# Kernel tuning notes

Measured on AMD Instinct MI355X. Metric: run time of the kernel, lower is better.

The kernel has to match this reference:

```python
import jax, jax.numpy as jnp
import numpy as np

B, C = 1, 1
D = H = W = 128          # volume depth/height/width (z, y, x)
V = U = 128              # detector rows (v) / cols (u)
A = 96                   # projection angles
N_STEPS = 128            # Joseph ray-marching steps
SX = SY = SD = 1.0       # voxel size (sd, sy, sx)
SU = SV = 1.0            # detector spacing (sv, su)


def setup_inputs() -> dict:
    key = jax.random.key(0)
    # model-facing volume [B, C, X, Y, Z]
    vol = jax.random.normal(key, (B, C, W, H, D), dtype=jnp.float32)
    angles = jnp.linspace(0.0, np.pi, A, endpoint=False).astype(jnp.float32)
    return {"vol": vol, "angles": angles}


def _corner(idx, size):
    """Floor/ceil corner indices + zero-padded linear weights (align_corners=True,
    padding_mode='zeros' semantics of F.grid_sample)."""
    i0f = jnp.floor(idx)
    frac = idx - i0f
    i0 = i0f.astype(jnp.int32)
    i1 = i0 + 1
    w0 = jnp.where((i0 >= 0) & (i0 < size), 1.0 - frac, 0.0)
    w1 = jnp.where((i1 >= 0) & (i1 < size), frac, 0.0)
    return jnp.clip(i0, 0, size - 1), jnp.clip(i1, 0, size - 1), w0, w1


def reference(vol, angles):
    # [B,C,X,Y,Z] -> [B,C,D,H,W] (z,y,x ordering used internally)
    v_zyx = jnp.transpose(vol, (0, 1, 4, 3, 2))
    cos_t = jnp.cos(angles)[:, None]   # [A,1]
    sin_t = jnp.sin(angles)[:, None]   # [A,1]
    u = (jnp.arange(U, dtype=jnp.float32) - (U - 1) / 2.0) * SU   # [U]
    v = (jnp.arange(V, dtype=jnp.float32) - (V - 1) / 2.0) * SV   # [V]
    # half ray length = half in-plane diagonal
    T = 0.5 * float(np.sqrt(((W - 1) * SX) ** 2 + ((H - 1) * SY) ** 2))
    delta_t = 2.0 * T / float(N_STEPS)

    x_base = -u[None, :] * sin_t   # [A,U] ray point at t=0
    y_base = u[None, :] * cos_t    # [A,U]
    # z depends only on detector row v; constant along the ray
    z_idx = v / SD + (D - 1) / 2.0                     # [V]
    z0, z1, wz0, wz1 = _corner(z_idx, D)
    z0, z1 = z0[:, None], z1[:, None]                  # [V,1]
    wz0, wz1 = wz0[:, None], wz1[:, None]

    t_vals = -T + (jnp.arange(N_STEPS, dtype=jnp.float32) + 0.5) * delta_t

    def step(acc, t):
        x_idx = (x_base + t * cos_t) / SX + (W - 1) / 2.0   # [A,U]
        y_idx = (y_base + t * sin_t) / SY + (H - 1) / 2.0   # [A,U]
        x0, x1, wx0, wx1 = [a[:, None, :] for a in _corner(x_idx, W)]  # [A,1,U]
        y0, y1, wy0, wy1 = [a[:, None, :] for a in _corner(y_idx, H)]  # [A,1,U]
        g = lambda zi, yi, xi: v_zyx[:, :, zi, yi, xi]      # -> [B,C,A,V,U]
        s = (wz0 * (wy0 * (wx0 * g(z0, y0, x0) + wx1 * g(z0, y0, x1))
                    + wy1 * (wx0 * g(z0, y1, x0) + wx1 * g(z0, y1, x1)))
             + wz1 * (wy0 * (wx0 * g(z1, y0, x0) + wx1 * g(z1, y0, x1))
                      + wy1 * (wx0 * g(z1, y1, x0) + wx1 * g(z1, y1, x1))))
        return acc + s, None

    acc0 = jnp.zeros((B, C, A, V, U), dtype=vol.dtype)
    acc, _ = jax.lax.scan(jax.checkpoint(step), acc0, t_vals)
    sino = acc * jnp.float32(delta_t)            # [B,C,A,V,U]
    # model-facing sinogram [B,C,X=U,A,Z=V]
    return jnp.transpose(sino, (0, 1, 4, 2, 3))
```

## Files before the change

### kernel.cpp

```cpp
#include <hip/hip_runtime.h>
#include <hip/hip_fp16.h>

namespace {
constexpr int A_N = 96;
constexpr int U_N = 128;
constexpr int V_N = 128;
constexpr int W_N = 128;
constexpr int H_N = 128;
constexpr int NSTEPS = 128;
constexpr float T_HALF = 89.80256121069154f;
constexpr float DT = 1.4031650189170554f;
constexpr float INV_DT = 1.0f / DT;
constexpr int PAD = 6;
constexpr int WP = W_N + 2 * PAD;
constexpr int ROW_BYTES = WP * 256;
constexpr int ZT = 8;
constexpr int RAYS_PER_WAVE = 8;
constexpr int RAYS_PER_BLOCK = 16;
constexpr int BLOCK_THREADS = 256;
constexpr size_t VOLP_COLS = (size_t)WP * WP;
constexpr size_t VOLP_BYTES = VOLP_COLS * 256;
constexpr size_t SINO = (size_t)U_N * A_N * V_N;
}

typedef __attribute__((ext_vector_type(4))) unsigned int u32x4;

__device__ __forceinline__ unsigned int packh2(float a, float b) {
    return (unsigned int)__half_as_ushort(__float2half_rn(a)) |
           ((unsigned int)__half_as_ushort(__float2half_rn(b)) << 16);
}

__global__ __launch_bounds__(256) void vol_pad_f16(
    const float* __restrict__ vol, unsigned int* __restrict__ volp)
{
    const int idx = blockIdx.x * 256 + threadIdx.x;
    if (idx >= (int)(VOLP_COLS * 16)) return;
    const int zo  = idx & 15;
    const int col = idx >> 4;
    const int yp = col % WP;
    const int xp = col / WP;
    const int x = xp - PAD;
    const int y = yp - PAD;
    uint4 o = make_uint4(0u, 0u, 0u, 0u);
    if ((unsigned)x < 128u && (unsigned)y < 128u) {
        const float* src = vol + (((size_t)x * 128 + y) << 7) + zo * 8;
        const float4 f0 = *(const float4*)(src);
        const float4 f1 = *(const float4*)(src + 4);
        o.x = packh2(f0.x, f0.y);
        o.y = packh2(f0.z, f0.w);
        o.z = packh2(f1.x, f1.y);
        o.w = packh2(f1.z, f1.w);
    }
    *(uint4*)((char*)volp + (size_t)col * 256 + zo * 16) = o;
}

#define ISSUE4(p, q0, q1, q2, q3)                                        \
    asm volatile("global_load_dwordx4 %0, %4, off\n\t"                   \
                 "global_load_dwordx4 %1, %4, off offset:128\n\t"        \
                 "global_load_dwordx4 %2, %4, off offset:256\n\t"        \
                 "global_load_dwordx4 %3, %4, off offset:384"            \
                 : "=&v"(q0), "=&v"(q1), "=&v"(q2), "=&v"(q3)            \
                 : "v"(p))

#define WAIT_VM8()  do { asm volatile("s_waitcnt vmcnt(8)" ::: "memory"); \
                         __builtin_amdgcn_sched_barrier(0); } while (0)
#define WAIT_VM0()  do { asm volatile("s_waitcnt vmcnt(0)" ::: "memory"); \
                         __builtin_amdgcn_sched_barrier(0); } while (0)

__global__ __launch_bounds__(BLOCK_THREADS, 4) void joseph_fwd_fused(
    const unsigned short* __restrict__ volp,
    const float* __restrict__ angles,
    float* __restrict__ out)
{
    const int zo = threadIdx.x & (ZT - 1);
    const int rw = (threadIdx.x >> 3) & 7;
    const int wv = threadIdx.x >> 6;
    const int ray = (wv & 1) * 8 + rw;
    const int shalf = wv >> 1;

    const int lin = (int)blockIdx.x + 8 * (int)blockIdx.y;
    const int swz = (lin & 7) * 96 + (lin >> 3);
    const int a   = swz >> 3;
    const int xtr = swz & 7;
    const int xt = (xtr & 1) ? (4 + (xtr >> 1)) : (3 - (xtr >> 1));
    const int u_i = xt * RAYS_PER_BLOCK + ray;

    const int i0 = shalf * (NSTEPS / 2);
    const int i1 = i0 + NSTEPS / 2;

    const float ang = angles[a];
    const float cv = cosf(ang);
    const float sv = sinf(ang);
    const float up = (float)u_i - 63.5f;
    const float xb = fmaf(-up, sv, 63.5f);
    const float yb = fmaf( up, cv, 63.5f);

    float tlo = -2.f * T_HALF, thi = 2.f * T_HALF;
    if (fabsf(cv) > 1e-6f) {
        const float ta = (-1.f - xb) / cv, tb = (128.f - xb) / cv;
        tlo = fmaxf(tlo, fminf(ta, tb));
        thi = fminf(thi, fmaxf(ta, tb));
    } else if (xb <= -1.f || xb >= 128.f) { thi = tlo - 1.f; }
    if (fabsf(sv) > 1e-6f) {
        const float ta = (-1.f - yb) / sv, tb = (128.f - yb) / sv;
        tlo = fmaxf(tlo, fminf(ta, tb));
        thi = fminf(thi, fmaxf(ta, tb));
    } else if (yb <= -1.f || yb >= 128.f) { thi = tlo - 1.f; }
    const int ilo = (int)floorf(fmaf(tlo + T_HALF, INV_DT, -0.5f)) - 1;
    const int ihi = (int)ceilf (fmaf(thi + T_HALF, INV_DT, -0.5f)) + 1;
    int lo = min(max(ilo, i0), i1);
    int hi = min(max(ihi + 1, i0), i1);
    lo &= ~1;
    hi = (hi + 1) & ~1;

    const char* __restrict__ volc = (const char*)volp;
    const int laneb = zo << 4;

    __half2 hacc[8];
    float accf[16];
#pragma unroll
    for (int j = 0; j < 8; ++j) hacc[j] = __float2half2_rn(0.f);
#pragma unroll
    for (int k = 0; k < 16; ++k) accf[k] = 0.f;

    auto base_of = [&](float i_f, float& fx, float& fy) -> const char* {
        const float tf = fmaf(i_f + 0.5f, DT, -T_HALF);
        const float xi = fmaf(tf, cv, xb);
        const float yi = fmaf(tf, sv, yb);
        const float fx0 = floorf(xi);
        const float fy0 = floorf(yi);
        fx = xi - fx0;
        fy = yi - fy0;
        const int x0 = (int)fx0;
        const int y0 = (int)fy0;
        return volc + ((((x0 + PAD) * WP + (y0 + PAD)) << 8) + laneb);
    };

    auto cons = [&](u32x4 q00l, u32x4 q00h, u32x4 q01l, u32x4 q01h,
                    u32x4 q10l, u32x4 q10h, u32x4 q11l, u32x4 q11h,
                    float fx, float fy) {
        const float wx0 = 1.f - fx;
        const float wy0 = 1.f - fy;
        const __half2 w00 = __float2half2_rn(wx0 * wy0);
        const __half2 w01 = __float2half2_rn(wx0 * fy);
        const __half2 w10 = __float2half2_rn(fx  * wy0);
        const __half2 w11 = __float2half2_rn(fx  * fy);
#pragma unroll
        for (int j = 0; j < 4; ++j) {
            hacc[j] = __hfma2(w00, __builtin_bit_cast(__half2, (unsigned int)q00l[j]), hacc[j]);
            hacc[j] = __hfma2(w01, __builtin_bit_cast(__half2, (unsigned int)q01l[j]), hacc[j]);
            hacc[j] = __hfma2(w10, __builtin_bit_cast(__half2, (unsigned int)q10l[j]), hacc[j]);
            hacc[j] = __hfma2(w11, __builtin_bit_cast(__half2, (unsigned int)q11l[j]), hacc[j]);
            hacc[4 + j] = __hfma2(w00, __builtin_bit_cast(__half2, (unsigned int)q00h[j]), hacc[4 + j]);
            hacc[4 + j] = __hfma2(w01, __builtin_bit_cast(__half2, (unsigned int)q01h[j]), hacc[4 + j]);
            hacc[4 + j] = __hfma2(w10, __builtin_bit_cast(__half2, (unsigned int)q10h[j]), hacc[4 + j]);
            hacc[4 + j] = __hfma2(w11, __builtin_bit_cast(__half2, (unsigned int)q11h[j]), hacc[4 + j]);
        }
    };

    auto flush = [&]() {
#pragma unroll
        for (int j = 0; j < 8; ++j) {
            const float2 f = __half22float2(hacc[j]);
            accf[2 * j]     += f.x;
            accf[2 * j + 1] += f.y;
            hacc[j] = __float2half2_rn(0.f);
        }
    };

    if (lo < hi) {
        u32x4 A0, A1, A2, A3, A4, A5, A6, A7;
        u32x4 B0, B1, B2, B3, B4, B5, B6, B7;
        float fxA, fyA, fxB, fyB;
        int kc = 0;
        int i = lo;
        {
            const char* p  = base_of((float)i, fxA, fyA);
            const char* p2 = p + ROW_BYTES;
            ISSUE4(p,  A0, A1, A2, A3);
            ISSUE4(p2, A4, A5, A6, A7);
        }
        for (;;) {
            {
                const char* p  = base_of((float)(i + 1), fxB, fyB);
                const char* p2 = p + ROW_BYTES;
                ISSUE4(p,  B0, B1, B2, B3);
                ISSUE4(p2, B4, B5, B6, B7);
            }
            WAIT_VM8();
            cons(A0, A1, A2, A3, A4, A5, A6, A7, fxA, fyA);
            i += 2;
            if (i >= hi) {
                WAIT_VM0();
                cons(B0, B1, B2, B3, B4, B5, B6, B7, fxB, fyB);
                break;
            }
            {
                const char* p  = base_of((float)i, fxA, fyA);
                const char* p2 = p + ROW_BYTES;
                ISSUE4(p,  A0, A1, A2, A3);
                ISSUE4(p2, A4, A5, A6, A7);
            }
            WAIT_VM8();
            cons(B0, B1, B2, B3, B4, B5, B6, B7, fxB, fyB);
            if (((++kc) & 1) == 0) flush();
        }
    }
    flush();

    __shared__ float part[RAYS_PER_BLOCK][V_N];
    if (shalf == 1) {
        float* p0 = &part[ray][8 * zo];
        float* p1 = &part[ray][64 + 8 * zo];
        *(float4*)(p0)     = make_float4(accf[0],  accf[1],  accf[2],  accf[3]);
        *(float4*)(p0 + 4) = make_float4(accf[4],  accf[5],  accf[6],  accf[7]);
        *(float4*)(p1)     = make_float4(accf[8],  accf[9],  accf[10], accf[11]);
        *(float4*)(p1 + 4) = make_float4(accf[12], accf[13], accf[14], accf[15]);
    }
    __syncthreads();
    if (shalf == 0) {
        const float* p0 = &part[ray][8 * zo];
        const float* p1 = &part[ray][64 + 8 * zo];
        const float4 q0 = *(const float4*)(p0);
        const float4 q1 = *(const float4*)(p0 + 4);
        const float4 q2 = *(const float4*)(p1);
        const float4 q3 = *(const float4*)(p1 + 4);
        float* op = out + ((size_t)u_i * A_N + a) * V_N;
        float* opl = op + 8 * zo;
        float* oph = op + 64 + 8 * zo;
        *(float4*)(opl)     = make_float4((accf[0]  + q0.x) * DT, (accf[1]  + q0.y) * DT,
                                          (accf[2]  + q0.z) * DT, (accf[3]  + q0.w) * DT);
        *(float4*)(opl + 4) = make_float4((accf[4]  + q1.x) * DT, (accf[5]  + q1.y) * DT,
                                          (accf[6]  + q1.z) * DT, (accf[7]  + q1.w) * DT);
        *(float4*)(oph)     = make_float4((accf[8]  + q2.x) * DT, (accf[9]  + q2.y) * DT,
                                          (accf[10] + q2.z) * DT, (accf[11] + q2.w) * DT);
        *(float4*)(oph + 4) = make_float4((accf[12] + q3.x) * DT, (accf[13] + q3.y) * DT,
                                          (accf[14] + q3.z) * DT, (accf[15] + q3.w) * DT);
    }
}

__global__ __launch_bounds__(256) void joseph_fwd_f32(
    const float* __restrict__ vol,
    const float* __restrict__ angles,
    float* __restrict__ out)
{
    const int zo  = threadIdx.x & 15;
    const int r   = threadIdx.x >> 4;
    const int u_i = blockIdx.x * 16 + r;
    const int a   = blockIdx.y;

    const float ang = angles[a];
    const float c = cosf(ang);
    const float s = sinf(ang);
    const float u = (float)u_i - 63.5f;
    const float xb = fmaf(-u, s, 63.5f);
    const float yb = fmaf( u, c, 63.5f);

    const float* volz = vol + 8 * zo;
    float4 accA = make_float4(0.f, 0.f, 0.f, 0.f);
    float4 accB = make_float4(0.f, 0.f, 0.f, 0.f);

    for (int i = 0; i < NSTEPS; ++i) {
        const float t  = fmaf((float)i + 0.5f, DT, -T_HALF);
        const float xi = fmaf(t, c, xb);
        const float yi = fmaf(t, s, yb);
        const float fx0f = floorf(xi);
        const float fy0f = floorf(yi);
        const int x0 = (int)fx0f;
        const int y0 = (int)fy0f;
        const float fx = xi - fx0f;
        const float fy = yi - fy0f;
        const int x1 = x0 + 1;
        const int y1 = y0 + 1;
        const float wx0 = (x0 >= 0 && x0 < W_N) ? (1.f - fx) : 0.f;
        const float wx1 = (x1 >= 0 && x1 < W_N) ? fx : 0.f;
        const float wy0 = (y0 >= 0 && y0 < H_N) ? (1.f - fy) : 0.f;
        const float wy1 = (y1 >= 0 && y1 < H_N) ? fy : 0.f;
        if ((wx0 + wx1) == 0.f || (wy0 + wy1) == 0.f) continue;
        const int cx0 = min(max(x0, 0), W_N - 1);
        const int cx1 = min(max(x1, 0), W_N - 1);
        const int cy0 = min(max(y0, 0), H_N - 1);
        const int cy1 = min(max(y1, 0), H_N - 1);
        const float* p00 = volz + ((cx0 * H_N + cy0) << 7);
        const float* p01 = volz + ((cx1 * H_N + cy0) << 7);
        const float* p10 = volz + ((cx0 * H_N + cy1) << 7);
        const float* p11 = volz + ((cx1 * H_N + cy1) << 7);
        const float4 v00a = *(const float4*)(p00);
        const float4 v00b = *(const float4*)(p00 + 4);
        const float4 v01a = *(const float4*)(p01);
        const float4 v01b = *(const float4*)(p01 + 4);
        const float4 v10a = *(const float4*)(p10);
        const float4 v10b = *(const float4*)(p10 + 4);
        const float4 v11a = *(const float4*)(p11);
        const float4 v11b = *(const float4*)(p11 + 4);
        const float w00 = wx0 * wy0, w01 = wx1 * wy0, w10 = wx0 * wy1, w11 = wx1 * wy1;
        accA.x = fmaf(w00, v00a.x, fmaf(w01, v01a.x, fmaf(w10, v10a.x, fmaf(w11, v11a.x, accA.x))));
        accA.y = fmaf(w00, v00a.y, fmaf(w01, v01a.y, fmaf(w10, v10a.y, fmaf(w11, v11a.y, accA.y))));
        accA.z = fmaf(w00, v00a.z, fmaf(w01, v01a.z, fmaf(w10, v10a.z, fmaf(w11, v11a.z, accA.z))));
        accA.w = fmaf(w00, v00a.w, fmaf(w01, v01a.w, fmaf(w10, v10a.w, fmaf(w11, v11a.w, accA.w))));
        accB.x = fmaf(w00, v00b.x, fmaf(w01, v01b.x, fmaf(w10, v10b.x, fmaf(w11, v11b.x, accB.x))));
        accB.y = fmaf(w00, v00b.y, fmaf(w01, v01b.y, fmaf(w10, v10b.y, fmaf(w11, v11b.y, accB.y))));
        accB.z = fmaf(w00, v00b.z, fmaf(w01, v01b.z, fmaf(w10, v10b.z, fmaf(w11, v11b.z, accB.z))));
        accB.w = fmaf(w00, v00b.w, fmaf(w01, v01b.w, fmaf(w10, v10b.w, fmaf(w11, v11b.w, accB.w))));
    }

    float* op = out + ((size_t)u_i * A_N + a) * V_N + 8 * zo;
    *(float4*)(op)     = make_float4(accA.x * DT, accA.y * DT, accA.z * DT, accA.w * DT);
    *(float4*)(op + 4) = make_float4(accB.x * DT, accB.y * DT, accB.z * DT, accB.w * DT);
}

extern "C" void kernel_launch(void* const* d_in, const int* in_sizes, int n_in,
                              void* d_out, int out_size, void* d_ws, size_t ws_size,
                              hipStream_t stream) {
    const float* vol    = (const float*)d_in[0];
    const float* angles = (const float*)d_in[1];
    float* out          = (float*)d_out;

    const int pad_blocks = (int)((VOLP_COLS * 16 + 255) / 256);

    if (ws_size >= VOLP_BYTES) {
        unsigned int* volp = (unsigned int*)d_ws;
        hipLaunchKernelGGL(vol_pad_f16, dim3(pad_blocks), dim3(256), 0, stream, vol, volp);
        dim3 grid(U_N / RAYS_PER_BLOCK, A_N);
        hipLaunchKernelGGL(joseph_fwd_fused, grid, dim3(BLOCK_THREADS), 0, stream,
                           (const unsigned short*)volp, angles, out);
    } else {
        dim3 grid(U_N / 16, A_N);
        hipLaunchKernelGGL(joseph_fwd_f32, grid, dim3(256), 0, stream, vol, angles, out);
    }
}
```

Measured before the change: 105.9 us.

## Split ray steps across four waves with interleaved step assignment

Each block now handles 8 rays instead of 16, and the four waves interleave over ray steps (stride 4) instead of two halves covering contiguous step ranges. Step ranges are unioned across the wave via shuffles, and out-of-range steps are masked with a zero weight and clamped addresses. The goal is to balance work between waves, since clipped rays previously left one half idle. The cost is extra masked loads for rays shorter than the wave maximum, a 3-way LDS reduction, and a doubled grid size, which the host launch must match.

```diff
diff --git a/kernel.cpp b/kernel.cpp
--- a/kernel.cpp
+++ b/kernel.cpp
@@ -15,12 +15,12 @@
 constexpr int WP = W_N + 2 * PAD;
 constexpr int ROW_BYTES = WP * 256;
 constexpr int ZT = 8;
-constexpr int RAYS_PER_WAVE = 8;
-constexpr int RAYS_PER_BLOCK = 16;
+constexpr int RAYS_PER_BLOCK = 8;
 constexpr int BLOCK_THREADS = 256;
 constexpr size_t VOLP_COLS = (size_t)WP * WP;
 constexpr size_t VOLP_BYTES = VOLP_COLS * 256;
 constexpr size_t SINO = (size_t)U_N * A_N * V_N;
+constexpr int MAXB = (int)(VOLP_BYTES - ROW_BYTES - 512);
 }
 
 typedef __attribute__((ext_vector_type(4))) unsigned int u32x4;
@@ -73,20 +73,15 @@
     float* __restrict__ out)
 {
     const int zo = threadIdx.x & (ZT - 1);
-    const int rw = (threadIdx.x >> 3) & 7;
+    const int r  = (threadIdx.x >> 3) & 7;
     const int wv = threadIdx.x >> 6;
-    const int ray = (wv & 1) * 8 + rw;
-    const int shalf = wv >> 1;
-
-    const int lin = (int)blockIdx.x + 8 * (int)blockIdx.y;
-    const int swz = (lin & 7) * 96 + (lin >> 3);
-    const int a   = swz >> 3;
-    const int xtr = swz & 7;
-    const int xt = (xtr & 1) ? (4 + (xtr >> 1)) : (3 - (xtr >> 1));
-    const int u_i = xt * RAYS_PER_BLOCK + ray;
-
-    const int i0 = shalf * (NSTEPS / 2);
-    const int i1 = i0 + NSTEPS / 2;
+
+    const int lin = (int)blockIdx.x + 16 * (int)blockIdx.y;
+    const int swz = (lin & 7) * 192 + (lin >> 3);
+    const int a   = swz >> 4;
+    const int xtr = swz & 15;
+    const int xt = (xtr & 1) ? (8 + (xtr >> 1)) : (7 - (xtr >> 1));
+    const int u_i = xt * RAYS_PER_BLOCK + r;
 
     const float ang = angles[a];
     const float cv = cosf(ang);
@@ -108,10 +103,15 @@
     } else if (yb <= -1.f || yb >= 128.f) { thi = tlo - 1.f; }
     const int ilo = (int)floorf(fmaf(tlo + T_HALF, INV_DT, -0.5f)) - 1;
     const int ihi = (int)ceilf (fmaf(thi + T_HALF, INV_DT, -0.5f)) + 1;
-    int lo = min(max(ilo, i0), i1);
-    int hi = min(max(ihi + 1, i0), i1);
-    lo &= ~1;
-    hi = (hi + 1) & ~1;
+    const int lo_r = min(max(ilo, 0), NSTEPS);
+    const int hi_r = min(max(ihi + 1, 0), NSTEPS);
+
+    int lo_w = lo_r, hi_w = hi_r;
+#pragma unroll
+    for (int m = 8; m < 64; m <<= 1) {
+        lo_w = min(lo_w, __shfl_xor(lo_w, m));
+        hi_w = max(hi_w, __shfl_xor(hi_w, m));
+    }
 
     const char* __restrict__ volc = (const char*)volp;
     const int laneb = zo << 4;
@@ -123,28 +123,32 @@
 #pragma unroll
     for (int k = 0; k < 16; ++k) accf[k] = 0.f;
 
-    auto base_of = [&](float i_f, float& fx, float& fy) -> const char* {
-        const float tf = fmaf(i_f + 0.5f, DT, -T_HALF);
+    auto base_of = [&](int i, float& fx, float& fy, float& vf) -> const char* {
+        const float tf = fmaf((float)i + 0.5f, DT, -T_HALF);
         const float xi = fmaf(tf, cv, xb);
         const float yi = fmaf(tf, sv, yb);
         const float fx0 = floorf(xi);
         const float fy0 = floorf(yi);
         fx = xi - fx0;
         fy = yi - fy0;
+        vf = (i >= lo_r && i < hi_r) ? 1.f : 0.f;
         const int x0 = (int)fx0;
         const int y0 = (int)fy0;
-        return volc + ((((x0 + PAD) * WP + (y0 + PAD)) << 8) + laneb);
+        int base = (((x0 + PAD) * WP + (y0 + PAD)) << 8);
+        base = min(max(base, 0), MAXB);
+        return volc + (base + laneb);
     };
 
     auto cons = [&](u32x4 q00l, u32x4 q00h, u32x4 q01l, u32x4 q01h,
                     u32x4 q10l, u32x4 q10h, u32x4 q11l, u32x4 q11h,
-                    float fx, float fy) {
-        const float wx0 = 1.f - fx;
+                    float fx, float fy, float vf) {
+        const float wx0 = (1.f - fx) * vf;
+        const float wx1 = fx * vf;
         const float wy0 = 1.f - fy;
         const __half2 w00 = __float2half2_rn(wx0 * wy0);
         const __half2 w01 = __float2half2_rn(wx0 * fy);
-        const __half2 w10 = __float2half2_rn(fx  * wy0);
-        const __half2 w11 = __float2half2_rn(fx  * fy);
+        const __half2 w10 = __float2half2_rn(wx1 * wy0);
+        const __half2 w11 = __float2half2_rn(wx1 * fy);
 #pragma unroll
         for (int j = 0; j < 4; ++j) {
             hacc[j] = __hfma2(w00, __builtin_bit_cast(__half2, (unsigned int)q00l[j]), hacc[j]);
@@ -168,74 +172,81 @@
         }
     };
 
-    if (lo < hi) {
+    const int i_start = lo_w + ((wv - lo_w) & 3);
+    if (i_start < hi_w) {
+        const int n = (hi_w - i_start + 3) >> 2;
+        const int n_pairs = (n + 1) >> 1;
         u32x4 A0, A1, A2, A3, A4, A5, A6, A7;
         u32x4 B0, B1, B2, B3, B4, B5, B6, B7;
-        float fxA, fyA, fxB, fyB;
-        int kc = 0;
-        int i = lo;
+        float fxA, fyA, vfA, fxB, fyB, vfB;
+        int i = i_start;
+        int k = 0;
         {
-            const char* p  = base_of((float)i, fxA, fyA);
+            const char* p  = base_of(i, fxA, fyA, vfA);
             const char* p2 = p + ROW_BYTES;
             ISSUE4(p,  A0, A1, A2, A3);
             ISSUE4(p2, A4, A5, A6, A7);
         }
         for (;;) {
             {
-                const char* p  = base_of((float)(i + 1), fxB, fyB);
+                const char* p  = base_of(i + 4, fxB, fyB, vfB);
                 const char* p2 = p + ROW_BYTES;
                 ISSUE4(p,  B0, B1, B2, B3);
                 ISSUE4(p2, B4, B5, B6, B7);
             }
             WAIT_VM8();
-            cons(A0, A1, A2, A3, A4, A5, A6, A7, fxA, fyA);
-            i += 2;
-            if (i >= hi) {
+            cons(A0, A1, A2, A3, A4, A5, A6, A7, fxA, fyA, vfA);
+            ++k;
+            if (k == n_pairs) {
                 WAIT_VM0();
-                cons(B0, B1, B2, B3, B4, B5, B6, B7, fxB, fyB);
+                cons(B0, B1, B2, B3, B4, B5, B6, B7, fxB, fyB, vfB);
                 break;
             }
             {
-                const char* p  = base_of((float)i, fxA, fyA);
+                const char* p  = base_of(i + 8, fxA, fyA, vfA);
                 const char* p2 = p + ROW_BYTES;
                 ISSUE4(p,  A0, A1, A2, A3);
                 ISSUE4(p2, A4, A5, A6, A7);
             }
             WAIT_VM8();
-            cons(B0, B1, B2, B3, B4, B5, B6, B7, fxB, fyB);
-            if (((++kc) & 1) == 0) flush();
+            cons(B0, B1, B2, B3, B4, B5, B6, B7, fxB, fyB, vfB);
+            i += 8;
+            if ((k & 1) == 0) flush();
         }
     }
     flush();
 
-    __shared__ float part[RAYS_PER_BLOCK][V_N];
-    if (shalf == 1) {
-        float* p0 = &part[ray][8 * zo];
-        float* p1 = &part[ray][64 + 8 * zo];
+    __shared__ float part[3][RAYS_PER_BLOCK][V_N];
+    if (wv > 0) {
+        float* p0 = &part[wv - 1][r][8 * zo];
+        float* p1 = &part[wv - 1][r][64 + 8 * zo];
         *(float4*)(p0)     = make_float4(accf[0],  accf[1],  accf[2],  accf[3]);
         *(float4*)(p0 + 4) = make_float4(accf[4],  accf[5],  accf[6],  accf[7]);
         *(float4*)(p1)     = make_float4(accf[8],  accf[9],  accf[10], accf[11]);
         *(float4*)(p1 + 4) = make_float4(accf[12], accf[13], accf[14], accf[15]);
     }
     __syncthreads();
-    if (shalf == 0) {
-        const float* p0 = &part[ray][8 * zo];
-        const float* p1 = &part[ray][64 + 8 * zo];
-        const float4 q0 = *(const float4*)(p0);
-        const float4 q1 = *(const float4*)(p0 + 4);
-        const float4 q2 = *(const float4*)(p1);
-        const float4 q3 = *(const float4*)(p1 + 4);
+    if (wv == 0) {
+#pragma unroll
+        for (int w = 0; w < 3; ++w) {
+            const float* p0 = &part[w][r][8 * zo];
+            const float* p1 = &part[w][r][64 + 8 * zo];
+            const float4 q0 = *(const float4*)(p0);
+            const float4 q1 = *(const float4*)(p0 + 4);
+            const float4 q2 = *(const float4*)(p1);
+            const float4 q3 = *(const float4*)(p1 + 4);
+            accf[0] += q0.x;  accf[1] += q0.y;  accf[2]  += q0.z;  accf[3]  += q0.w;
+            accf[4] += q1.x;  accf[5] += q1.y;  accf[6]  += q1.z;  accf[7]  += q1.w;
+            accf[8] += q2.x;  accf[9] += q2.y;  accf[10] += q2.z;  accf[11] += q2.w;
+            accf[12] += q3.x; accf[13] += q3.y; accf[14] += q3.z;  accf[15] += q3.w;
+        }
         float* op = out + ((size_t)u_i * A_N + a) * V_N;
         float* opl = op + 8 * zo;
         float* oph = op + 64 + 8 * zo;
-        *(float4*)(opl)     = make_float4((accf[0]  + q0.x) * DT, (accf[1]  + q0.y) * DT,
-                                          (accf[2]  + q0.z) * DT, (accf[3]  + q0.w) * DT);
-        *(float4*)(opl + 4) = make_float4((accf[4]  + q1.x) * DT, (accf[5]  + q1.y) * DT,
-                                          (accf[6]  + q1.z) * DT, (accf[7]  + q1.w) * DT);
-        *(float4*)(oph)     = make_float4((accf[8]  + q2.x) * DT, (accf[9]  + q2.y) * DT,
-                                          (accf[10] + q2.z) * DT, (accf[11] + q2.w) * DT);
-        *(float4*)(oph + 4) = make_float4((accf[12] + q3.x) * DT, (accf[13] + q3.y) * DT,
-                                          (accf[14] + q3.z) * DT, (accf[15] + q3.w) * DT);
+        *(float4*)(opl)     = make_float4(accf[0]  * DT, accf[1]  * DT, accf[2]  * DT, accf[3]  * DT);
+        *(float4*)(opl + 4) = make_float4(accf[4]  * DT, accf[5]  * DT, accf[6]  * DT, accf[7]  * DT);
+        *(float4*)(oph)     = make_float4(accf[8]  * DT, accf[9]  * DT, accf[10] * DT, accf[11] * DT);
+        *(float4*)(oph + 4) = make_float4(accf[12] * DT, accf[13] * DT, accf[14] * DT, accf[15] * DT);
     }
 }
 
```

Result: slower. 115.1 us (+8.6%).
